# Kernel optimization log

Measured on AMD Instinct MI355X. Metric: run time of the kernel, lower is better.

Reference implementation:

```python
import jax, jax.numpy as jnp
import numpy as np

EMB = 768
HEADS = 4
HEAD_DIM = EMB // HEADS


def setup_inputs() -> dict:
    key = jax.random.key(0)
    ks = jax.random.split(key, 11)
    B, S = 8, 2048
    scale = 1.0 / np.sqrt(EMB)
    inp = {
        "q": jax.random.normal(ks[0], (B, S, EMB), dtype=jnp.float32),
        "k": jax.random.normal(ks[1], (B, S, EMB), dtype=jnp.float32),
        "v": jax.random.normal(ks[2], (B, S, EMB), dtype=jnp.float32),
        "Wq": jax.random.normal(ks[3], (EMB, EMB), dtype=jnp.float32) * scale,
        "bq": jnp.zeros((EMB,), dtype=jnp.float32),
        "Wk": jax.random.normal(ks[4], (EMB, EMB), dtype=jnp.float32) * scale,
        "bk": jnp.zeros((EMB,), dtype=jnp.float32),
        "Wv": jax.random.normal(ks[5], (EMB, EMB), dtype=jnp.float32) * scale,
        "bv": jnp.zeros((EMB,), dtype=jnp.float32),
        "Wo": jax.random.normal(ks[6], (EMB, EMB), dtype=jnp.float32) * scale,
        "bo": jnp.zeros((EMB,), dtype=jnp.float32),
    }
    return inp


def reference(q, k, v, Wq, bq, Wk, bk, Wv, bv, Wo, bo):
    B, S, _ = q.shape
    # Linear projections (torch Linear: x @ W.T + b)
    Q = q @ Wq.T + bq
    K = k @ Wk.T + bk
    V = v @ Wv.T + bv
    # split heads: [B, H, S, Dh]
    def split(x):
        return x.reshape(B, S, HEADS, HEAD_DIM).transpose(0, 2, 1, 3)
    Qh, Kh, Vh = split(Q), split(K), split(V)
    # energy [B, H, S, S]; note: original's mask_fill is a non-inplace no-op, so no masking
    energy = jnp.einsum("bhqd,bhkd->bhqk", Qh, Kh)
    att = jax.nn.softmax(energy / jnp.sqrt(jnp.float32(HEAD_DIM)), axis=-1)
    # dropout p=0 -> identity
    out = jnp.einsum("bhqk,bhkd->bhqd", att, Vh)
    out = out.transpose(0, 2, 1, 3).reshape(B, S, EMB)
    return out @ Wo.T + bo
```

## Files before the change

### kernel.cpp

```cpp
#include <hip/hip_runtime.h>
#include <hip/hip_bf16.h>
#include <cstdint>
#include <cstddef>

#define EMB   768
#define HEADS 4
#define HD    192
#define BATCH 8
#define SEQ   2048
#define MROWS (BATCH * SEQ)

typedef __attribute__((ext_vector_type(8))) short bf16x8;
typedef __attribute__((ext_vector_type(4))) float f32x4;

#define GLOBAL_AS __attribute__((address_space(1)))
#define LDS_AS    __attribute__((address_space(3)))

__device__ __forceinline__ void async16(unsigned short* lds, const unsigned short* g) {
    __builtin_amdgcn_global_load_lds((const GLOBAL_AS void*)g, (LDS_AS void*)lds, 16, 0, 0);
}

__device__ __forceinline__ unsigned short f2bf(float f) {
    union { float f; unsigned int u; } v; v.f = f;
    unsigned int u = v.u;
    unsigned int r = u + 0x7fffu + ((u >> 16) & 1u);
    return (unsigned short)(r >> 16);
}

__device__ __forceinline__ unsigned long long pack4bf(float4 f) {
    union { __hip_bfloat162 h; unsigned int u; } a, b;
    a.h = __float22bfloat162_rn(make_float2(f.x, f.y));
    b.h = __float22bfloat162_rn(make_float2(f.z, f.w));
    return (unsigned long long)a.u | ((unsigned long long)b.u << 32);
}

__device__ __forceinline__ int swz(int colbyte, int row) {
    return colbyte ^ ((row & 7) << 4);
}

__global__ __launch_bounds__(256) void conv_kernel(
    const float* __restrict__ x, unsigned short* __restrict__ y, int n4)
{
    int i = blockIdx.x * 256 + threadIdx.x;
    int stride = gridDim.x * 256;
    for (; i < n4; i += stride) {
        float4 f = ((const float4*)x)[i];
        ((unsigned long long*)y)[i] = pack4bf(f);
    }
}

__global__ __launch_bounds__(256) void conv3_kernel(
    const float* __restrict__ a, const float* __restrict__ b,
    const float* __restrict__ c, unsigned short* __restrict__ y, int n4)
{
    int i = blockIdx.x * 256 + threadIdx.x;
    int stride = gridDim.x * 256;
    for (; i < 3 * n4; i += stride) {
        int sel = i / n4, off = i - sel * n4;
        const float* s = (sel == 0) ? a : (sel == 1) ? b : c;
        float4 f = ((const float4*)s)[off];
        ((unsigned long long*)y)[i] = pack4bf(f);
    }
}

#define GEMM_PROLOG                                                          \
    const int tid  = threadIdx.x;                                            \
    const int wg   = (blockIdx.x & 7) * 96 + (blockIdx.x >> 3);              \
    const int n0   = (wg % 6) * 128;                                         \
    const int m0   = (wg / 6) * 128;                                         \
    const int w    = tid >> 6;                                               \
    const int lane = tid & 63;                                               \
    const int l15  = lane & 15;                                              \
    const int quad = lane >> 4;                                              \
    const int wm   = (w >> 1) * 64;                                          \
    const int wn   = (w & 1) * 64;                                           \
    const int arow = lane >> 2;           \
    const int acol = (lane & 3) * 8;                  \
    f32x4 acc[4][4];                                                         \
    _Pragma("unroll")                                                        \
    for (int a = 0; a < 4; a++)                                              \
        _Pragma("unroll")                                                    \
        for (int b = 0; b < 4; b++) acc[a][b] = (f32x4)0.0f;

#define GEMM_STAGE(buf, Aptr, Bptr, k0)                                      \
    _Pragma("unroll")                                                        \
    for (int j = 0; j < 2; j++) {                                            \
        int r = w * 32 + j * 16 + arow;                                      \
        async16(&Al[(buf) * 4096 + (w * 2 + j) * 512],                       \
                Aptr + (size_t)(m0 + r) * 768 + (k0) + acol);                \
        async16(&Bl[(buf) * 4096 + (w * 2 + j) * 512],                       \
                Bptr + (size_t)(n0 + r) * 768 + (k0) + acol);                \
    }

#define GEMM_COMPUTE(buf)                                                    \
    {                                                                        \
        bf16x8 af[4], bfr[4];                                                \
        _Pragma("unroll")                                                    \
        for (int mi = 0; mi < 4; mi++)                                       \
            af[mi] = *(const bf16x8*)&Al[(buf) * 4096 +                      \
                                         (wm + mi * 16 + l15) * 32 + quad * 8]; \
        _Pragma("unroll")                                                    \
        for (int ni = 0; ni < 4; ni++)                                       \
            bfr[ni] = *(const bf16x8*)&Bl[(buf) * 4096 +                     \
                                          (wn + ni * 16 + l15) * 32 + quad * 8]; \
        _Pragma("unroll")                                                    \
        for (int mi = 0; mi < 4; mi++)                                       \
            _Pragma("unroll")                                                \
            for (int ni = 0; ni < 4; ni++)                                   \
                acc[mi][ni] = __builtin_amdgcn_mfma_f32_16x16x32_bf16(       \
                    af[mi], bfr[ni], acc[mi][ni], 0, 0, 0);                  \
    }

#define GEMM_KLOOP(Aptr, Bptr)                                               \
    GEMM_STAGE(0, Aptr, Bptr, 0)                                             \
    for (int k0 = 0; k0 < 768; k0 += 64) {                                   \
        __syncthreads();                                                     \
        GEMM_STAGE(1, Aptr, Bptr, k0 + 32)                                   \
        GEMM_COMPUTE(0)                                                      \
        __syncthreads();                                                     \
        if (k0 + 64 < 768) { GEMM_STAGE(0, Aptr, Bptr, k0 + 64) }            \
        GEMM_COMPUTE(1)                                                      \
    }

__global__ __launch_bounds__(256) void proj_kernel(
    const unsigned short* __restrict__ X,
    const unsigned short* __restrict__ Wb,
    const float* __restrict__ bias,
    unsigned short* __restrict__ out,
    float scale)
{
    __shared__ __align__(16) unsigned short smem[16384];
    unsigned short* Al = smem;
    unsigned short* Bl = smem + 8192;
    GEMM_PROLOG
    GEMM_KLOOP(X, Wb)

    const int b = m0 >> 11;
#pragma unroll
    for (int mi = 0; mi < 4; mi++) {
#pragma unroll
        for (int ni = 0; ni < 4; ni++) {
            int jj = n0 + wn + ni * 16 + l15;
            int h  = jj / HD;
            int d  = jj - h * HD;
            float bj = bias[jj];
#pragma unroll
            for (int r = 0; r < 4; r++) {
                int i = m0 + wm + mi * 16 + quad * 4 + r;
                int s = i & (SEQ - 1);
                out[(size_t)((b * HEADS + h) * SEQ + s) * HD + d] =
                    f2bf((acc[mi][ni][r] + bj) * scale);
            }
        }
    }
}

__global__ __launch_bounds__(256) void vproj_kernel(
    const unsigned short* __restrict__ X,
    const unsigned short* __restrict__ Wb,
    const float* __restrict__ bias,
    unsigned short* __restrict__ out)
{
    __shared__ __align__(16) unsigned short smem[16384];
    unsigned short* Al = smem;
    unsigned short* Bl = smem + 8192;
    GEMM_PROLOG
    GEMM_KLOOP(X, Wb)

    __syncthreads();
    unsigned short* Tl = smem;
    const int batch = m0 >> 11;
    const int s0    = m0 & (SEQ - 1);

#pragma unroll
    for (int g = 0; g < 4; g++) {
        if ((w & 1) == (g >> 1)) {
#pragma unroll
            for (int t = 0; t < 2; t++) {
                int ni = (g & 1) * 2 + t;
                int jj = n0 + (w & 1) * 64 + ni * 16 + l15;
                int dl = t * 16 + l15;
                float bj = bias[jj];
#pragma unroll
                for (int mi = 0; mi < 4; mi++)
#pragma unroll
                    for (int r = 0; r < 4; r++)
                        Tl[dl * 136 + wm + mi * 16 + quad * 4 + r] =
                            f2bf(acc[mi][ni][r] + bj);
            }
        }
        __syncthreads();
#pragma unroll
        for (int t = 0; t < 2; t++) {
            int u  = tid + t * 256;
            int dl = u >> 4;
            int cg = u & 15;
            int jj = n0 + g * 32 + dl;
            int hh = jj / HD;
            int d  = jj - hh * HD;
            *(int4*)(out + ((size_t)((batch * HEADS + hh) * HD + d)) * SEQ + s0 + cg * 8) =
                *(const int4*)&Tl[dl * 136 + cg * 8];
        }
        __syncthreads();
    }
}

__global__ __launch_bounds__(256) void oproj_kernel(
    const unsigned short* __restrict__ A,
    const unsigned short* __restrict__ Wb,
    const float* __restrict__ bias,
    float* __restrict__ out)
{
    __shared__ __align__(16) unsigned short smem[16384];
    unsigned short* Al = smem;
    unsigned short* Bl = smem + 8192;
    GEMM_PROLOG
    GEMM_KLOOP(A, Wb)

#pragma unroll
    for (int mi = 0; mi < 4; mi++) {
#pragma unroll
        for (int ni = 0; ni < 4; ni++) {
            int jj = n0 + wn + ni * 16 + l15;
            float bj = bias[jj];
#pragma unroll
            for (int r = 0; r < 4; r++) {
                int i = m0 + wm + mi * 16 + quad * 4 + r;
                out[(size_t)i * 768 + jj] = acc[mi][ni][r] + bj;
            }
        }
    }
}

__global__ __launch_bounds__(256, 2) void attn_kernel(
    const unsigned short* __restrict__ Q,
    const unsigned short* __restrict__ K,
    const unsigned short* __restrict__ Vt,
    unsigned short* __restrict__ O)
{
    __shared__ __align__(16) unsigned short Kl[64 * 192];
    __shared__ __align__(16) unsigned short Vl[192 * 64];
    __shared__ __align__(16) unsigned short Pl[4 * 32 * 64];

    const int tid  = threadIdx.x;
    const int w    = tid >> 6;
    const int lane = tid & 63;
    const int l15  = lane & 15;
    const int quad = lane >> 4;
    const int flat = blockIdx.x;
    const int loc  = flat >> 3;
    const int bh   = (flat & 7) * 4 + (loc >> 4);
    const int qt   = loc & 15;
    const int b    = bh >> 2;
    const int h    = bh & 3;
    const size_t kbase = (size_t)bh * SEQ * HD;

    bf16x8 qf[2][6];
    {
        const unsigned short* qp =
            Q + kbase + (size_t)(qt * 128 + w * 32 + l15) * HD + quad * 8;
#pragma unroll
        for (int mg = 0; mg < 2; mg++)
#pragma unroll
            for (int kk = 0; kk < 6; kk++)
                qf[mg][kk] = *(const bf16x8*)(qp + mg * 16 * HD + kk * 32);
    }

#pragma unroll
    for (int i = 0; i < 6; i++) {
        int u = tid + i * 256;
        int row = u / 24, rem = u - row * 24;
        int cgp = rem ^ (row & 7);
        async16(&Kl[(i * 256 + w * 64) * 8],
                K + kbase + (size_t)row * HD + cgp * 8);
    }

    f32x4 oacc[2][12];
#pragma unroll
    for (int mg = 0; mg < 2; mg++)
#pragma unroll
        for (int i = 0; i < 12; i++) oacc[mg][i] = (f32x4)0.0f;
    float lacc[2][4] = {{0.f, 0.f, 0.f, 0.f}, {0.f, 0.f, 0.f, 0.f}};

    for (int kt = 0; kt < SEQ / 64; kt++) {
        __syncthreads();

#pragma unroll
        for (int i = 0; i < 6; i++) {
            int u = tid + i * 256;
            int row = u >> 3;
            int cgp = (u & 7) ^ (row & 7);
            async16(&Vl[(i * 256 + w * 64) * 8],
                    Vt + kbase + (size_t)row * SEQ + kt * 64 + cgp * 8);
        }

        f32x4 sacc[2][4];
#pragma unroll
        for (int mg = 0; mg < 2; mg++)
#pragma unroll
            for (int nj = 0; nj < 4; nj++) sacc[mg][nj] = (f32x4)0.0f;

        __builtin_amdgcn_s_setprio(1);
#pragma unroll
        for (int kk = 0; kk < 6; kk++) {
#pragma unroll
            for (int nj = 0; nj < 4; nj++) {
                int row = nj * 16 + l15;
                bf16x8 bfr = *(const bf16x8*)((const char*)Kl + row * 384 +
                                              swz(kk * 64 + quad * 16, row));
                sacc[0][nj] = __builtin_amdgcn_mfma_f32_16x16x32_bf16(
                    qf[0][kk], bfr, sacc[0][nj], 0, 0, 0);
                sacc[1][nj] = __builtin_amdgcn_mfma_f32_16x16x32_bf16(
                    qf[1][kk], bfr, sacc[1][nj], 0, 0, 0);
            }
        }
        __builtin_amdgcn_s_setprio(0);

        {
            char* pw = (char*)Pl + w * 4096;
#pragma unroll
            for (int mg = 0; mg < 2; mg++)
#pragma unroll
                for (int nj = 0; nj < 4; nj++) {
                    int colb = (nj * 16 + l15) * 2;
#pragma unroll
                    for (int r = 0; r < 4; r++) {
                        float pv = __expf(sacc[mg][nj][r]);
                        lacc[mg][r] += pv;
                        int row = mg * 16 + quad * 4 + r;
                        *(unsigned short*)(pw + row * 128 + swz(colb, row)) = f2bf(pv);
                    }
                }
        }

        __syncthreads();

        {
            int ktn = (kt + 1) & (SEQ / 64 - 1);
#pragma unroll
            for (int i = 0; i < 6; i++) {
                int u = tid + i * 256;
                int row = u / 24, rem = u - row * 24;
                int cgp = rem ^ (row & 7);
                async16(&Kl[(i * 256 + w * 64) * 8],
                        K + kbase + (size_t)(ktn * 64 + row) * HD + cgp * 8);
            }
        }

#pragma unroll
        for (int kk = 0; kk < 2; kk++) {
            const char* pr = (const char*)Pl + w * 4096;
            bf16x8 pa0 = *(const bf16x8*)(pr + l15 * 128 + swz(kk * 64 + quad * 16, l15));
            bf16x8 pa1 = *(const bf16x8*)(pr + (16 + l15) * 128 + swz(kk * 64 + quad * 16, 16 + l15));
            __builtin_amdgcn_s_setprio(1);
#pragma unroll
            for (int nf = 0; nf < 12; nf++) {
                int vrow = nf * 16 + l15;
                bf16x8 vb = *(const bf16x8*)((const char*)Vl + vrow * 128 +
                                             swz(kk * 64 + quad * 16, vrow));
                oacc[0][nf] = __builtin_amdgcn_mfma_f32_16x16x32_bf16(pa0, vb, oacc[0][nf], 0, 0, 0);
                oacc[1][nf] = __builtin_amdgcn_mfma_f32_16x16x32_bf16(pa1, vb, oacc[1][nf], 0, 0, 0);
            }
            __builtin_amdgcn_s_setprio(0);
        }
    }

    float inv[2][4];
#pragma unroll
    for (int mg = 0; mg < 2; mg++)
#pragma unroll
        for (int r = 0; r < 4; r++) {
            float lsum = lacc[mg][r];
#pragma unroll
            for (int off = 1; off < 16; off <<= 1)
                lsum += __shfl_xor(lsum, off, 64);
            inv[mg][r] = 1.0f / lsum;
        }
#pragma unroll
    for (int mg = 0; mg < 2; mg++)
#pragma unroll
        for (int nf = 0; nf < 12; nf++) {
            int col = h * HD + nf * 16 + l15;
#pragma unroll
            for (int r = 0; r < 4; r++) {
                int s = qt * 128 + w * 32 + mg * 16 + quad * 4 + r;
                O[(size_t)(b * SEQ + s) * EMB + col] = f2bf(oacc[mg][nf][r] * inv[mg][r]);
            }
        }
}

extern "C" void kernel_launch(void* const* d_in, const int* in_sizes, int n_in,
                              void* d_out, int out_size, void* d_ws, size_t ws_size,
                              hipStream_t stream)
{
    const float* q  = (const float*)d_in[0];
    const float* k  = (const float*)d_in[1];
    const float* v  = (const float*)d_in[2];
    const float* Wq = (const float*)d_in[3];
    const float* bq = (const float*)d_in[4];
    const float* Wk = (const float*)d_in[5];
    const float* bk = (const float*)d_in[6];
    const float* Wv = (const float*)d_in[7];
    const float* bv = (const float*)d_in[8];
    const float* Wo = (const float*)d_in[9];
    const float* bo = (const float*)d_in[10];
    float* out = (float*)d_out;

    unsigned short* Xbf = (unsigned short*)d_out;
    unsigned short* S   = (unsigned short*)d_ws;
    unsigned short* Qb  = S  + (size_t)MROWS * EMB;
    unsigned short* Kb  = Qb + (size_t)MROWS * EMB;
    unsigned short* Vb  = Kb + (size_t)MROWS * EMB;
    const size_t WSZ = (size_t)EMB * EMB;

    const float scl = 0.07216878364870323f;
    const int   nx4 = MROWS * EMB / 4;
    const int   nw4 = EMB * EMB / 4;

    dim3 pb(256);
    dim3 pg(768);
    dim3 cgx(4096), cgw(576);

    conv3_kernel<<<dim3(1728), pb, 0, stream>>>(Wq, Wk, Wv, S, nw4);

    conv_kernel<<<cgx, pb, 0, stream>>>(q, Xbf, nx4);
    proj_kernel<<<pg, pb, 0, stream>>>(Xbf, S, bq, Qb, scl);

    conv_kernel<<<cgx, pb, 0, stream>>>(k, Xbf, nx4);
    proj_kernel<<<pg, pb, 0, stream>>>(Xbf, S + WSZ, bk, Kb, 1.0f);

    conv_kernel<<<cgx, pb, 0, stream>>>(v, Xbf, nx4);
    vproj_kernel<<<pg, pb, 0, stream>>>(Xbf, S + 2 * WSZ, bv, Vb);

    dim3 ag(512);
    attn_kernel<<<ag, pb, 0, stream>>>(Qb, Kb, Vb, S);

    conv_kernel<<<cgw, pb, 0, stream>>>(Wo, Qb, nw4);
    oproj_kernel<<<pg, pb, 0, stream>>>(S, Qb, bo, out);
}
```

Measured before the change: 475.7 us.

## Fuse fp32-to-bf16 input conversion into a single merged QKV projection kernel

The three separate activation conversion passes and three projection launches become one kernel. It reads fp32 activations directly, packs them to bf16 in registers and writes them into LDS, while the weights still stream in asynchronously. The grid covers all three projections with an XCD-aware block mapping, and the V transpose epilogue is selected per block. This removes the round trips that wrote and re-read bf16 copies of the activations and cuts launch count, at the cost of synchronous global loads for A that may hide latency less well.

```diff
diff --git a/kernel.cpp b/kernel.cpp
--- a/kernel.cpp
+++ b/kernel.cpp
@@ -32,6 +32,13 @@
     a.h = __float22bfloat162_rn(make_float2(f.x, f.y));
     b.h = __float22bfloat162_rn(make_float2(f.z, f.w));
     return (unsigned long long)a.u | ((unsigned long long)b.u << 32);
+}
+
+__device__ __forceinline__ int4 pack8bf(float4 lo, float4 hi) {
+    union { unsigned long long u[2]; int4 i; } r;
+    r.u[0] = pack4bf(lo);
+    r.u[1] = pack4bf(hi);
+    return r.i;
 }
 
 __device__ __forceinline__ int swz(int colbyte, int row) {
@@ -122,86 +129,144 @@
         GEMM_COMPUTE(1)                                                      \
     }
 
-__global__ __launch_bounds__(256) void proj_kernel(
-    const unsigned short* __restrict__ X,
-    const unsigned short* __restrict__ Wb,
-    const float* __restrict__ bias,
-    unsigned short* __restrict__ out,
-    float scale)
+#define PROJ_A_LOAD(k0)                                                      \
+    {                                                                        \
+        const float* pa = X + (size_t)(m0 + w * 32 + arow) * 768 + (k0) + acol; \
+        a0 = *(const float4*)pa;  a1 = *(const float4*)(pa + 4);             \
+        a2 = *(const float4*)(pa + 16 * 768);                                \
+        a3 = *(const float4*)(pa + 16 * 768 + 4);                            \
+    }
+
+#define PROJ_A_WRITE(buf)                                                    \
+    {                                                                        \
+        *(int4*)&Al[(buf) * 4096 + (w * 2 + 0) * 512 + lane * 8] = pack8bf(a0, a1); \
+        *(int4*)&Al[(buf) * 4096 + (w * 2 + 1) * 512 + lane * 8] = pack8bf(a2, a3); \
+    }
+
+#define PROJ_B_STAGE(buf, k0)                                                \
+    _Pragma("unroll")                                                        \
+    for (int j = 0; j < 2; j++) {                                            \
+        int r = w * 32 + j * 16 + arow;                                      \
+        async16(&Bl[(buf) * 4096 + (w * 2 + j) * 512],                       \
+                Wb + (size_t)(n0 + r) * 768 + (k0) + acol);                  \
+    }
+
+__global__ __launch_bounds__(256) void projqkv_kernel(
+    const float* __restrict__ Xq, const float* __restrict__ Xk,
+    const float* __restrict__ Xv,
+    const unsigned short* __restrict__ Wall,
+    const float* __restrict__ bqp, const float* __restrict__ bkp,
+    const float* __restrict__ bvp,
+    unsigned short* __restrict__ Qo, unsigned short* __restrict__ Ko,
+    unsigned short* __restrict__ Vo)
 {
     __shared__ __align__(16) unsigned short smem[16384];
     unsigned short* Al = smem;
     unsigned short* Bl = smem + 8192;
-    GEMM_PROLOG
-    GEMM_KLOOP(X, Wb)
-
-    const int b = m0 >> 11;
-#pragma unroll
-    for (int mi = 0; mi < 4; mi++) {
-#pragma unroll
-        for (int ni = 0; ni < 4; ni++) {
-            int jj = n0 + wn + ni * 16 + l15;
-            int h  = jj / HD;
-            int d  = jj - h * HD;
-            float bj = bias[jj];
-#pragma unroll
-            for (int r = 0; r < 4; r++) {
-                int i = m0 + wm + mi * 16 + quad * 4 + r;
-                int s = i & (SEQ - 1);
-                out[(size_t)((b * HEADS + h) * SEQ + s) * HD + d] =
-                    f2bf((acc[mi][ni][r] + bj) * scale);
-            }
-        }
-    }
-}
-
-__global__ __launch_bounds__(256) void vproj_kernel(
-    const unsigned short* __restrict__ X,
-    const unsigned short* __restrict__ Wb,
-    const float* __restrict__ bias,
-    unsigned short* __restrict__ out)
-{
-    __shared__ __align__(16) unsigned short smem[16384];
-    unsigned short* Al = smem;
-    unsigned short* Bl = smem + 8192;
-    GEMM_PROLOG
-    GEMM_KLOOP(X, Wb)
-
-    __syncthreads();
-    unsigned short* Tl = smem;
-    const int batch = m0 >> 11;
-    const int s0    = m0 & (SEQ - 1);
-
-#pragma unroll
-    for (int g = 0; g < 4; g++) {
-        if ((w & 1) == (g >> 1)) {
+
+    const int tid  = threadIdx.x;
+    const int flat = blockIdx.x;
+    const int xcd  = flat & 7;
+    const int loc  = flat >> 3;
+    const int sel  = loc / 96;
+    const int wg   = xcd * 96 + (loc - sel * 96);
+    const int n0   = (wg % 6) * 128;
+    const int m0   = (wg / 6) * 128;
+    const int w    = tid >> 6;
+    const int lane = tid & 63;
+    const int l15  = lane & 15;
+    const int quad = lane >> 4;
+    const int wm   = (w >> 1) * 64;
+    const int wn   = (w & 1) * 64;
+    const int arow = lane >> 2;
+    const int acol = (lane & 3) * 8;
+
+    const float* X = (sel == 0) ? Xq : (sel == 1) ? Xk : Xv;
+    const unsigned short* Wb = Wall + (size_t)sel * (EMB * EMB);
+    const float* bias = (sel == 0) ? bqp : (sel == 1) ? bkp : bvp;
+    const float scale = (sel == 0) ? 0.07216878364870323f : 1.0f;
+
+    f32x4 acc[4][4];
+#pragma unroll
+    for (int a = 0; a < 4; a++)
+#pragma unroll
+        for (int b = 0; b < 4; b++) acc[a][b] = (f32x4)0.0f;
+
+    float4 a0, a1, a2, a3;
+
+    PROJ_A_LOAD(0)
+    PROJ_B_STAGE(0, 0)
+    PROJ_A_WRITE(0)
+
+    for (int k0 = 0; k0 < 768; k0 += 64) {
+        __syncthreads();
+        PROJ_A_LOAD(k0 + 32)
+        PROJ_B_STAGE(1, k0 + 32)
+        GEMM_COMPUTE(0)
+        PROJ_A_WRITE(1)
+        __syncthreads();
+        bool more = (k0 + 64) < 768;
+        if (more) { PROJ_A_LOAD(k0 + 64) PROJ_B_STAGE(0, k0 + 64) }
+        GEMM_COMPUTE(1)
+        if (more) { PROJ_A_WRITE(0) }
+    }
+
+    if (sel < 2) {
+        unsigned short* out = (sel == 0) ? Qo : Ko;
+        const int b = m0 >> 11;
+#pragma unroll
+        for (int mi = 0; mi < 4; mi++) {
+#pragma unroll
+            for (int ni = 0; ni < 4; ni++) {
+                int jj = n0 + wn + ni * 16 + l15;
+                int h  = jj / HD;
+                int d  = jj - h * HD;
+                float bj = bias[jj];
+#pragma unroll
+                for (int r = 0; r < 4; r++) {
+                    int i = m0 + wm + mi * 16 + quad * 4 + r;
+                    int s = i & (SEQ - 1);
+                    out[(size_t)((b * HEADS + h) * SEQ + s) * HD + d] =
+                        f2bf((acc[mi][ni][r] + bj) * scale);
+                }
+            }
+        }
+    } else {
+        __syncthreads();
+        unsigned short* Tl = smem;
+        const int batch = m0 >> 11;
+        const int s0    = m0 & (SEQ - 1);
+#pragma unroll
+        for (int g = 0; g < 4; g++) {
+            if ((w & 1) == (g >> 1)) {
+#pragma unroll
+                for (int t = 0; t < 2; t++) {
+                    int ni = (g & 1) * 2 + t;
+                    int jj = n0 + (w & 1) * 64 + ni * 16 + l15;
+                    int dl = t * 16 + l15;
+                    float bj = bias[jj];
+#pragma unroll
+                    for (int mi = 0; mi < 4; mi++)
+#pragma unroll
+                        for (int r = 0; r < 4; r++)
+                            Tl[dl * 136 + wm + mi * 16 + quad * 4 + r] =
+                                f2bf(acc[mi][ni][r] + bj);
+                }
+            }
+            __syncthreads();
 #pragma unroll
             for (int t = 0; t < 2; t++) {
-                int ni = (g & 1) * 2 + t;
-                int jj = n0 + (w & 1) * 64 + ni * 16 + l15;
-                int dl = t * 16 + l15;
-                float bj = bias[jj];
-#pragma unroll
-                for (int mi = 0; mi < 4; mi++)
-#pragma unroll
-                    for (int r = 0; r < 4; r++)
-                        Tl[dl * 136 + wm + mi * 16 + quad * 4 + r] =
-                            f2bf(acc[mi][ni][r] + bj);
-            }
-        }
-        __syncthreads();
-#pragma unroll
-        for (int t = 0; t < 2; t++) {
-            int u  = tid + t * 256;
-            int dl = u >> 4;
-            int cg = u & 15;
-            int jj = n0 + g * 32 + dl;
-            int hh = jj / HD;
-            int d  = jj - hh * HD;
-            *(int4*)(out + ((size_t)((batch * HEADS + hh) * HD + d)) * SEQ + s0 + cg * 8) =
-                *(const int4*)&Tl[dl * 136 + cg * 8];
-        }
-        __syncthreads();
+                int u  = tid + t * 256;
+                int dl = u >> 4;
+                int cg = u & 15;
+                int jj = n0 + g * 32 + dl;
+                int hh = jj / HD;
+                int d  = jj - hh * HD;
+                *(int4*)(Vo + ((size_t)((batch * HEADS + hh) * HD + d)) * SEQ + s0 + cg * 8) =
+                    *(const int4*)&Tl[dl * 136 + cg * 8];
+            }
+            __syncthreads();
+        }
     }
 }
 
@@ -406,35 +471,18 @@
     const float* bo = (const float*)d_in[10];
     float* out = (float*)d_out;
 
-    unsigned short* Xbf = (unsigned short*)d_out;
     unsigned short* S   = (unsigned short*)d_ws;
     unsigned short* Qb  = S  + (size_t)MROWS * EMB;
     unsigned short* Kb  = Qb + (size_t)MROWS * EMB;
     unsigned short* Vb  = Kb + (size_t)MROWS * EMB;
-    const size_t WSZ = (size_t)EMB * EMB;
-
-    const float scl = 0.07216878364870323f;
-    const int   nx4 = MROWS * EMB / 4;
-    const int   nw4 = EMB * EMB / 4;
-
+
+    const int nw4 = EMB * EMB / 4;
     dim3 pb(256);
-    dim3 pg(768);
-    dim3 cgx(4096), cgw(576);
 
     conv3_kernel<<<dim3(1728), pb, 0, stream>>>(Wq, Wk, Wv, S, nw4);
-
-    conv_kernel<<<cgx, pb, 0, stream>>>(q, Xbf, nx4);
-    proj_kernel<<<pg, pb, 0, stream>>>(Xbf, S, bq, Qb, scl);
-
-    conv_kernel<<<cgx, pb, 0, stream>>>(k, Xbf, nx4);
-    proj_kernel<<<pg, pb, 0, stream>>>(Xbf, S + WSZ, bk, Kb, 1.0f);
-
-    conv_kernel<<<cgx, pb, 0, stream>>>(v, Xbf, nx4);
-    vproj_kernel<<<pg, pb, 0, stream>>>(Xbf, S + 2 * WSZ, bv, Vb);
-
-    dim3 ag(512);
-    attn_kernel<<<ag, pb, 0, stream>>>(Qb, Kb, Vb, S);
-
-    conv_kernel<<<cgw, pb, 0, stream>>>(Wo, Qb, nw4);
-    oproj_kernel<<<pg, pb, 0, stream>>>(S, Qb, bo, out);
-}
+    projqkv_kernel<<<dim3(2304), pb, 0, stream>>>(q, k, v, S, bq, bk, bv,
+                                                  Qb, Kb, Vb);
+    attn_kernel<<<dim3(512), pb, 0, stream>>>(Qb, Kb, Vb, S);
+    conv_kernel<<<dim3(576), pb, 0, stream>>>(Wo, Qb, nw4);
+    oproj_kernel<<<dim3(768), pb, 0, stream>>>(S, Qb, bo, out);
+}
```

Measured after the change: 482.6 us. Within noise of the previous version (+1.5%).
